# Optimization experiments

Hardware: AMD Instinct MI355X
Metric: run time of the kernel (lower is better)

Reference implementation:

```python
import jax, jax.numpy as jnp
import numpy as np

LEFT, RIGHT = 64, 64  # left_size, right_size; hidden = LEFT*RIGHT = 4096


def _cayley(raw):
    """torch nn.utils.parametrizations.orthogonal(..., orthogonal_map='cayley',
    use_trivialization=False): A = triu(raw, 1); X = A - A^T (skew-symmetric);
    Q = (I - X/2)^{-1} (I + X/2)."""
    n = raw.shape[0]
    A = jnp.triu(raw, 1)
    X = A - A.T
    Id = jnp.eye(n, dtype=raw.dtype)
    return jnp.linalg.solve(Id - 0.5 * X, Id + 0.5 * X)


def setup_inputs() -> dict:
    key = jax.random.key(0)
    ks = jax.random.split(key, 8)
    B, S = 4, 2048
    H = LEFT * RIGHT
    inp = jax.random.normal(ks[0], (B, S, H), dtype=jnp.float32)
    raw_u_left = jax.random.normal(ks[1], (LEFT, LEFT), dtype=jnp.float32) * 0.02
    raw_v_left = jax.random.normal(ks[2], (LEFT, LEFT), dtype=jnp.float32) * 0.02
    raw_u_right = jax.random.normal(ks[3], (RIGHT, RIGHT), dtype=jnp.float32) * 0.02
    raw_v_right = jax.random.normal(ks[4], (RIGHT, RIGHT), dtype=jnp.float32) * 0.02
    diag_left = jnp.ones((LEFT,), dtype=jnp.float32)
    diag_right = jnp.ones((RIGHT,), dtype=jnp.float32)
    diag_scale = jnp.ones((H,), dtype=jnp.float32) + 0.01 * jax.random.normal(ks[5], (H,), dtype=jnp.float32)
    return {
        "inp": inp,
        "raw_u_left": raw_u_left,
        "raw_v_left": raw_v_left,
        "diag_left": diag_left,
        "raw_u_right": raw_u_right,
        "raw_v_right": raw_v_right,
        "diag_right": diag_right,
        "diag_scale": diag_scale,
        "inv_t": 0,
    }


def reference(inp, raw_u_left, raw_v_left, diag_left, raw_u_right, raw_v_right,
              diag_right, diag_scale, inv_t):
    # add_diag=True, use_diag=True path
    if inv_t:
        x = inp / diag_scale
        dl = 1.0 / diag_left
        dr = 1.0 / diag_right
    else:
        x = inp * diag_scale
        dl = diag_left
        dr = diag_right
    # Cayley-parametrized orthogonal factors
    Ul = _cayley(raw_u_left)
    Vl = _cayley(raw_v_left)
    Ur = _cayley(raw_u_right)
    Vr = _cayley(raw_v_right)
    # SVD-style reconstruction: M = U @ diag(d) @ V^T
    ML = (Ul * dl[None, :]) @ Vl.T  # [LEFT, LEFT]
    MR = (Ur * dr[None, :]) @ Vr.T  # [RIGHT, RIGHT]
    # Kronecker matmul: view last dim as [LEFT, RIGHT], out = ML^T @ X @ MR
    orig_shape = x.shape
    xb = x.reshape(-1, LEFT, RIGHT)  # [B*S, LEFT, RIGHT]
    out = jnp.einsum('bij,ik,jl->bkl', xb, ML, MR)
    return out.reshape(orig_shape)
```

## Files before the change

### kernel.cpp

```cpp
#include <hip/hip_runtime.h>
#include <hip/hip_bf16.h>

typedef short short8 __attribute__((ext_vector_type(8)));
typedef short short4v __attribute__((ext_vector_type(4)));
typedef float f32x4 __attribute__((ext_vector_type(4)));
typedef float f32x16 __attribute__((ext_vector_type(16)));

#define HID 4096
#define CST 68

__device__ __forceinline__ unsigned short f2bf(float f) {
    unsigned int u = __float_as_uint(f);
    u = (u + 0x7FFFu + ((u >> 16) & 1u)) >> 16;
    return (unsigned short)u;
}

__device__ __forceinline__ f32x4 mm4(const float* SA, const float* SB, int i, int j0) {
    f32x4 acc = {0.f, 0.f, 0.f, 0.f};
#pragma unroll 8
    for (int k = 0; k < 64; ++k) {
        float a = SA[i * CST + k];
        acc += a * *reinterpret_cast<const f32x4*>(SB + k * CST + j0);
    }
    return acc;
}

__global__ __launch_bounds__(1024) void cayley_build_kernel(
    const float* __restrict__ rul, const float* __restrict__ rvl, const float* __restrict__ dl,
    const float* __restrict__ rur, const float* __restrict__ rvr, const float* __restrict__ dr,
    const int* __restrict__ invt,
    unsigned short* __restrict__ plb, unsigned short* __restrict__ mrtb)
{
    __shared__ __align__(16) float Yw[64 * CST], Aw[64 * CST], Pw[64 * CST];
    __shared__ __align__(16) float Qw[64 * CST], QTw[64 * CST];
    __shared__ float dd[64];

    const float* ru; const float* rv; const float* dv; unsigned short* ob;
    if (blockIdx.x == 0) { ru = rul; rv = rvl; dv = dl; ob = plb; }
    else                 { ru = rur; rv = rvr; dv = dr; ob = mrtb; }

    const int tid = threadIdx.x;
    const int i = tid >> 4;
    const int j0 = (tid & 15) << 2;

    for (int pass = 0; pass < 2; ++pass) {
        const float* raw = (pass == 0) ? ru : rv;
#pragma unroll
        for (int q = 0; q < 4; ++q) {
            int j = j0 + q;
            float v = 0.f;
            if (j > i)      v =  raw[i * 64 + j];
            else if (j < i) v = -raw[j * 64 + i];
            Yw[i * CST + j] = 0.5f * v;
        }
        __syncthreads();
        f32x4 a = mm4(Yw, Yw, i, j0);
        __syncthreads();
        *reinterpret_cast<f32x4*>(Aw + i * CST + j0) = a;
        *reinterpret_cast<f32x4*>(Pw + i * CST + j0) =
            a + *reinterpret_cast<const f32x4*>(Yw + i * CST + j0);
        __syncthreads();
        a = mm4(Pw, Aw, i, j0);
        __syncthreads();
        *reinterpret_cast<f32x4*>(Pw + i * CST + j0) += a;
        __syncthreads();
        a = mm4(Aw, Aw, i, j0);
        __syncthreads();
        *reinterpret_cast<f32x4*>(Aw + i * CST + j0) = a;
        __syncthreads();
        a = mm4(Pw, Aw, i, j0);
        __syncthreads();
        f32x4 p = *reinterpret_cast<const f32x4*>(Pw + i * CST + j0) + a;
#pragma unroll
        for (int q = 0; q < 4; ++q) {
            int j = j0 + q;
            float qv = ((i == j) ? 1.f : 0.f) + 2.f * p[q];
            if (pass == 0) Qw[i * CST + j]  = qv;
            else           QTw[j * CST + i] = qv;
        }
        __syncthreads();
    }
    if (tid < 64) { float d = dv[tid]; dd[tid] = (invt[0] != 0) ? (1.0f / d) : d; }
    __syncthreads();

    f32x4 m = {0.f, 0.f, 0.f, 0.f};
#pragma unroll 8
    for (int j = 0; j < 64; ++j) {
        float aa = Qw[i * CST + j] * dd[j];
        m += aa * *reinterpret_cast<const f32x4*>(QTw + j * CST + j0);
    }
#pragma unroll
    for (int q = 0; q < 4; ++q)
        ob[(j0 + q) * 64 + i] = f2bf(m[q]);
}

__global__ __launch_bounds__(256, 4) void kron_kernel(
    const float* __restrict__ inp, const float* __restrict__ ds,
    const unsigned short* __restrict__ plb, const unsigned short* __restrict__ mrtb,
    const int* __restrict__ invt, float* __restrict__ out, int ntok)
{
    __shared__ __align__(16) unsigned char sbuf[4][8192];
    const int w = threadIdx.x >> 6;
    const int lane = threadIdx.x & 63;
    const int r = lane & 31;
    const int h = lane >> 5;
    unsigned char* S = sbuf[w];

    const int t = blockIdx.x * 4 + w;
    if (t >= ntok) return;
    const bool inv = (invt[0] != 0);

    const float* xt = inp + (size_t)t * HID;
    const int c = lane & 7;
    const int mr0 = lane >> 3;
#pragma unroll
    for (int s = 0; s < 8; ++s) {
        const int fi = s * 512 + lane * 8;
        f32x4 x0 = *reinterpret_cast<const f32x4*>(xt + fi);
        f32x4 x1 = *reinterpret_cast<const f32x4*>(xt + fi + 4);
        f32x4 d0 = *reinterpret_cast<const f32x4*>(ds + fi);
        f32x4 d1 = *reinterpret_cast<const f32x4*>(ds + fi + 4);
        if (inv) {
#pragma unroll
            for (int e = 0; e < 4; ++e) { x0[e] /= d0[e]; x1[e] /= d1[e]; }
        } else {
            x0 *= d0; x1 *= d1;
        }
        short8 f;
#pragma unroll
        for (int e = 0; e < 4; ++e) {
            f[e]     = (short)f2bf(x0[e]);
            f[e + 4] = (short)f2bf(x1[e]);
        }
        const int m = s * 8 + mr0;
        *reinterpret_cast<short8*>(S + ((m * 8 + (c ^ (m & 7))) << 4)) = f;
    }
    asm volatile("s_waitcnt lgkmcnt(0)" ::: "memory");
    __builtin_amdgcn_sched_barrier(0);

    short8 a1[2][4];
#pragma unroll
    for (int mt = 0; mt < 2; ++mt)
#pragma unroll
        for (int kt = 0; kt < 4; ++kt)
            a1[mt][kt] = *reinterpret_cast<const short8*>(
                S + (((32 * mt + r) * 8 + ((2 * kt + h) ^ (r & 7))) << 4));
    short8 b1[4][2];
#pragma unroll
    for (int kt = 0; kt < 4; ++kt)
#pragma unroll
        for (int nt = 0; nt < 2; ++nt)
            b1[kt][nt] = *reinterpret_cast<const short8*>(
                (const short*)mrtb + (32 * nt + r) * 64 + 16 * kt + 8 * h);

    asm volatile("s_waitcnt lgkmcnt(0)" ::: "memory");
    __builtin_amdgcn_sched_barrier(0);

#pragma unroll
    for (int mt = 0; mt < 2; ++mt)
#pragma unroll
        for (int nt = 0; nt < 2; ++nt) {
            f32x16 acc = {0.f};
#pragma unroll
            for (int kt = 0; kt < 4; ++kt)
                acc = __builtin_amdgcn_mfma_f32_32x32x16_bf16(a1[mt][kt], b1[kt][nt], acc, 0, 0, 0);
            const int l = 32 * nt + r;
#pragma unroll
            for (int q = 0; q < 4; ++q) {
                short4v zz;
#pragma unroll
                for (int e = 0; e < 4; ++e) zz[e] = (short)f2bf(acc[4 * q + e]);
                *reinterpret_cast<short4v*>(
                    S + (((l * 8 + ((4 * mt + q) ^ (l & 7))) << 4) + 8 * h)) = zz;
            }
        }
    asm volatile("s_waitcnt lgkmcnt(0)" ::: "memory");
    __builtin_amdgcn_sched_barrier(0);

    short8 b2[4][2];
#pragma unroll
    for (int kt = 0; kt < 4; ++kt)
#pragma unroll
        for (int nt = 0; nt < 2; ++nt)
            b2[kt][nt] = *reinterpret_cast<const short8*>(
                S + (((32 * nt + r) * 8 + ((2 * kt + h) ^ (r & 7))) << 4));
    short8 a2[2][4];
#pragma unroll
    for (int mt = 0; mt < 2; ++mt)
#pragma unroll
        for (int kt = 0; kt < 4; ++kt)
            a2[mt][kt] = *reinterpret_cast<const short8*>(
                (const short*)plb + (32 * mt + r) * 64 + 16 * kt + 8 * h);

    float* op = out + (size_t)t * HID;
#pragma unroll
    for (int mt = 0; mt < 2; ++mt)
#pragma unroll
        for (int nt = 0; nt < 2; ++nt) {
            f32x16 acc = {0.f};
#pragma unroll
            for (int kt = 0; kt < 4; ++kt)
                acc = __builtin_amdgcn_mfma_f32_32x32x16_bf16(a2[mt][kt], b2[kt][nt], acc, 0, 0, 0);
#pragma unroll
            for (int g = 0; g < 16; ++g) {
                const int k = 32 * mt + (g & 3) + 8 * (g >> 2) + 4 * h;
                op[k * 64 + 32 * nt + r] = acc[g];
            }
        }
}

extern "C" void kernel_launch(void* const* d_in, const int* in_sizes, int n_in,
                              void* d_out, int out_size, void* d_ws, size_t ws_size,
                              hipStream_t stream) {
    const float* inp = (const float*)d_in[0];
    const float* rul = (const float*)d_in[1];
    const float* rvl = (const float*)d_in[2];
    const float* dl  = (const float*)d_in[3];
    const float* rur = (const float*)d_in[4];
    const float* rvr = (const float*)d_in[5];
    const float* dr  = (const float*)d_in[6];
    const float* ds  = (const float*)d_in[7];
    const int*   invt = (const int*)d_in[8];
    float* out = (float*)d_out;

    unsigned short* plb  = (unsigned short*)d_ws;
    unsigned short* mrtb = plb + 4096;

    const int ntok = in_sizes[0] / HID;

    hipLaunchKernelGGL(cayley_build_kernel, dim3(2), dim3(1024), 0, stream,
                       rul, rvl, dl, rur, rvr, dr, invt, plb, mrtb);
    const int nblk = (ntok + 3) / 4;
    hipLaunchKernelGGL(kron_kernel, dim3(nblk), dim3(256), 0, stream,
                       inp, ds, plb, mrtb, invt, out, ntok);
}
```

Measured before the change: 87.84 us.

## Stage output through swizzled LDS for coalesced stores, pre-pack weights, two tokens per wave

```diff
diff --git a/kernel.cpp b/kernel.cpp
--- a/kernel.cpp
+++ b/kernel.cpp
@@ -8,6 +8,11 @@
 
 #define HID 4096
 #define CST 68
+#define TPW 2
+#define WLDS 9216
+
+#define LGKM0 do { asm volatile("s_waitcnt lgkmcnt(0)" ::: "memory"); \
+                   __builtin_amdgcn_sched_barrier(0); } while (0)
 
 __device__ __forceinline__ unsigned short f2bf(float f) {
     unsigned int u = __float_as_uint(f);
@@ -29,15 +34,15 @@
     const float* __restrict__ rul, const float* __restrict__ rvl, const float* __restrict__ dl,
     const float* __restrict__ rur, const float* __restrict__ rvr, const float* __restrict__ dr,
     const int* __restrict__ invt,
-    unsigned short* __restrict__ plb, unsigned short* __restrict__ mrtb)
+    unsigned short* __restrict__ plp, unsigned short* __restrict__ mrp)
 {
     __shared__ __align__(16) float Yw[64 * CST], Aw[64 * CST], Pw[64 * CST];
     __shared__ __align__(16) float Qw[64 * CST], QTw[64 * CST];
     __shared__ float dd[64];
 
     const float* ru; const float* rv; const float* dv; unsigned short* ob;
-    if (blockIdx.x == 0) { ru = rul; rv = rvl; dv = dl; ob = plb; }
-    else                 { ru = rur; rv = rvr; dv = dr; ob = mrtb; }
+    if (blockIdx.x == 0) { ru = rul; rv = rvl; dv = dl; ob = plp; }
+    else                 { ru = rur; rv = rvr; dv = dr; ob = mrp; }
 
     const int tid = threadIdx.x;
     const int i = tid >> 4;
@@ -89,124 +94,148 @@
         float aa = Qw[i * CST + j] * dd[j];
         m += aa * *reinterpret_cast<const f32x4*>(QTw + j * CST + j0);
     }
-#pragma unroll
-    for (int q = 0; q < 4; ++q)
-        ob[(j0 + q) * 64 + i] = f2bf(m[q]);
+    const int kt = i >> 4, hh = (i >> 3) & 1, e = i & 7;
+#pragma unroll
+    for (int q = 0; q < 4; ++q) {
+        int j = j0 + q;
+        unsigned short v = f2bf(m[q]);
+        int dst;
+        if (blockIdx.x == 0)
+            dst = (((j >> 5) * 4 + kt) * 64 + (j & 31) + 32 * hh) * 8 + e;
+        else
+            dst = ((kt * 2 + (j >> 5)) * 64 + (j & 31) + 32 * hh) * 8 + e;
+        ob[dst] = v;
+    }
 }
 
 __global__ __launch_bounds__(256, 4) void kron_kernel(
     const float* __restrict__ inp, const float* __restrict__ ds,
-    const unsigned short* __restrict__ plb, const unsigned short* __restrict__ mrtb,
+    const unsigned short* __restrict__ plp, const unsigned short* __restrict__ mrp,
     const int* __restrict__ invt, float* __restrict__ out, int ntok)
 {
-    __shared__ __align__(16) unsigned char sbuf[4][8192];
+    __shared__ __align__(16) unsigned char sbuf[4][WLDS];
     const int w = threadIdx.x >> 6;
     const int lane = threadIdx.x & 63;
     const int r = lane & 31;
     const int h = lane >> 5;
     unsigned char* S = sbuf[w];
-
-    const int t = blockIdx.x * 4 + w;
-    if (t >= ntok) return;
+    float* SF = reinterpret_cast<float*>(S);
     const bool inv = (invt[0] != 0);
 
-    const float* xt = inp + (size_t)t * HID;
-    const int c = lane & 7;
-    const int mr0 = lane >> 3;
-#pragma unroll
-    for (int s = 0; s < 8; ++s) {
-        const int fi = s * 512 + lane * 8;
-        f32x4 x0 = *reinterpret_cast<const f32x4*>(xt + fi);
-        f32x4 x1 = *reinterpret_cast<const f32x4*>(xt + fi + 4);
-        f32x4 d0 = *reinterpret_cast<const f32x4*>(ds + fi);
-        f32x4 d1 = *reinterpret_cast<const f32x4*>(ds + fi + 4);
-        if (inv) {
-#pragma unroll
-            for (int e = 0; e < 4; ++e) { x0[e] /= d0[e]; x1[e] /= d1[e]; }
-        } else {
-            x0 *= d0; x1 *= d1;
-        }
-        short8 f;
-#pragma unroll
-        for (int e = 0; e < 4; ++e) {
-            f[e]     = (short)f2bf(x0[e]);
-            f[e + 4] = (short)f2bf(x1[e]);
-        }
-        const int m = s * 8 + mr0;
-        *reinterpret_cast<short8*>(S + ((m * 8 + (c ^ (m & 7))) << 4)) = f;
-    }
-    asm volatile("s_waitcnt lgkmcnt(0)" ::: "memory");
-    __builtin_amdgcn_sched_barrier(0);
-
-    short8 a1[2][4];
-#pragma unroll
-    for (int mt = 0; mt < 2; ++mt)
+    const int t0 = (blockIdx.x * 4 + w) * TPW;
+#pragma unroll
+    for (int it = 0; it < TPW; ++it) {
+        const int t = t0 + it;
+        if (t >= ntok) break;
+        const float* xt = inp + (size_t)t * HID;
+
+#pragma unroll
+        for (int s = 0; s < 8; ++s) {
+            const int fi = s * 512 + lane * 8;
+            f32x4 x0 = *reinterpret_cast<const f32x4*>(xt + fi);
+            f32x4 x1 = *reinterpret_cast<const f32x4*>(xt + fi + 4);
+            f32x4 d0 = *reinterpret_cast<const f32x4*>(ds + fi);
+            f32x4 d1 = *reinterpret_cast<const f32x4*>(ds + fi + 4);
+            if (inv) {
+#pragma unroll
+                for (int e = 0; e < 4; ++e) { x0[e] /= d0[e]; x1[e] /= d1[e]; }
+            } else {
+                x0 *= d0; x1 *= d1;
+            }
+            short8 f;
+#pragma unroll
+            for (int e = 0; e < 4; ++e) {
+                f[e]     = (short)f2bf(x0[e]);
+                f[e + 4] = (short)f2bf(x1[e]);
+            }
+            const int m = s * 8 + (lane >> 3);
+            const int c = lane & 7;
+            *reinterpret_cast<short8*>(S + ((m * 8 + (c ^ (m & 7))) << 4)) = f;
+        }
+        LGKM0;
+
+        short8 a1[8];
+#pragma unroll
+        for (int mt = 0; mt < 2; ++mt)
+#pragma unroll
+            for (int kt = 0; kt < 4; ++kt)
+                a1[mt * 4 + kt] = *reinterpret_cast<const short8*>(
+                    S + (((32 * mt + r) * 8 + ((2 * kt + h) ^ (r & 7))) << 4));
+        short8 b1[8];
 #pragma unroll
         for (int kt = 0; kt < 4; ++kt)
-            a1[mt][kt] = *reinterpret_cast<const short8*>(
-                S + (((32 * mt + r) * 8 + ((2 * kt + h) ^ (r & 7))) << 4));
-    short8 b1[4][2];
-#pragma unroll
-    for (int kt = 0; kt < 4; ++kt)
-#pragma unroll
-        for (int nt = 0; nt < 2; ++nt)
-            b1[kt][nt] = *reinterpret_cast<const short8*>(
-                (const short*)mrtb + (32 * nt + r) * 64 + 16 * kt + 8 * h);
-
-    asm volatile("s_waitcnt lgkmcnt(0)" ::: "memory");
-    __builtin_amdgcn_sched_barrier(0);
-
-#pragma unroll
-    for (int mt = 0; mt < 2; ++mt)
-#pragma unroll
-        for (int nt = 0; nt < 2; ++nt) {
-            f32x16 acc = {0.f};
+#pragma unroll
+            for (int nt = 0; nt < 2; ++nt)
+                b1[kt * 2 + nt] = *reinterpret_cast<const short8*>(
+                    mrp + ((kt * 2 + nt) * 64 + lane) * 8);
+        LGKM0;
+
+#pragma unroll
+        for (int mt = 0; mt < 2; ++mt)
+#pragma unroll
+            for (int nt = 0; nt < 2; ++nt) {
+                f32x16 acc = {0.f};
+#pragma unroll
+                for (int kt = 0; kt < 4; ++kt)
+                    acc = __builtin_amdgcn_mfma_f32_32x32x16_bf16(
+                        a1[mt * 4 + kt], b1[kt * 2 + nt], acc, 0, 0, 0);
+                const int l2 = 32 * nt + r;
+#pragma unroll
+                for (int q = 0; q < 4; ++q) {
+                    short4v zz;
+#pragma unroll
+                    for (int e = 0; e < 4; ++e) zz[e] = (short)f2bf(acc[4 * q + e]);
+                    *reinterpret_cast<short4v*>(
+                        S + (((l2 * 8 + ((4 * mt + q) ^ (l2 & 7))) << 4) + 8 * h)) = zz;
+                }
+            }
+        LGKM0;
+
+        short8 b2[8];
+#pragma unroll
+        for (int kt = 0; kt < 4; ++kt)
+#pragma unroll
+            for (int nt = 0; nt < 2; ++nt)
+                b2[kt * 2 + nt] = *reinterpret_cast<const short8*>(
+                    S + (((32 * nt + r) * 8 + ((2 * kt + h) ^ (r & 7))) << 4));
+        short8 a2[8];
+#pragma unroll
+        for (int mt = 0; mt < 2; ++mt)
 #pragma unroll
             for (int kt = 0; kt < 4; ++kt)
-                acc = __builtin_amdgcn_mfma_f32_32x32x16_bf16(a1[mt][kt], b1[kt][nt], acc, 0, 0, 0);
-            const int l = 32 * nt + r;
-#pragma unroll
-            for (int q = 0; q < 4; ++q) {
-                short4v zz;
-#pragma unroll
-                for (int e = 0; e < 4; ++e) zz[e] = (short)f2bf(acc[4 * q + e]);
-                *reinterpret_cast<short4v*>(
-                    S + (((l * 8 + ((4 * mt + q) ^ (l & 7))) << 4) + 8 * h)) = zz;
-            }
-        }
-    asm volatile("s_waitcnt lgkmcnt(0)" ::: "memory");
-    __builtin_amdgcn_sched_barrier(0);
-
-    short8 b2[4][2];
-#pragma unroll
-    for (int kt = 0; kt < 4; ++kt)
-#pragma unroll
-        for (int nt = 0; nt < 2; ++nt)
-            b2[kt][nt] = *reinterpret_cast<const short8*>(
-                S + (((32 * nt + r) * 8 + ((2 * kt + h) ^ (r & 7))) << 4));
-    short8 a2[2][4];
-#pragma unroll
-    for (int mt = 0; mt < 2; ++mt)
-#pragma unroll
-        for (int kt = 0; kt < 4; ++kt)
-            a2[mt][kt] = *reinterpret_cast<const short8*>(
-                (const short*)plb + (32 * mt + r) * 64 + 16 * kt + 8 * h);
-
-    float* op = out + (size_t)t * HID;
-#pragma unroll
-    for (int mt = 0; mt < 2; ++mt)
-#pragma unroll
-        for (int nt = 0; nt < 2; ++nt) {
-            f32x16 acc = {0.f};
-#pragma unroll
-            for (int kt = 0; kt < 4; ++kt)
-                acc = __builtin_amdgcn_mfma_f32_32x32x16_bf16(a2[mt][kt], b2[kt][nt], acc, 0, 0, 0);
-#pragma unroll
-            for (int g = 0; g < 16; ++g) {
-                const int k = 32 * mt + (g & 3) + 8 * (g >> 2) + 4 * h;
-                op[k * 64 + 32 * nt + r] = acc[g];
-            }
-        }
+                a2[mt * 4 + kt] = *reinterpret_cast<const short8*>(
+                    plp + ((mt * 4 + kt) * 64 + lane) * 8);
+        LGKM0;
+
+        float* op = out + (size_t)t * HID;
+#pragma unroll
+        for (int mt = 0; mt < 2; ++mt) {
+#pragma unroll
+            for (int nt = 0; nt < 2; ++nt) {
+                f32x16 acc = {0.f};
+#pragma unroll
+                for (int kt = 0; kt < 4; ++kt)
+                    acc = __builtin_amdgcn_mfma_f32_32x32x16_bf16(
+                        a2[mt * 4 + kt], b2[kt * 2 + nt], acc, 0, 0, 0);
+#pragma unroll
+                for (int g = 0; g < 16; ++g) {
+                    const int rr = (g & 3) + 8 * (g >> 2) + 4 * h;
+                    const int cy = 32 * nt + r;
+                    SF[rr * 68 + (cy ^ ((rr & 7) << 2))] = acc[g];
+                }
+            }
+            LGKM0;
+#pragma unroll
+            for (int s = 0; s < 8; ++s) {
+                const int ro = s * 4 + (lane >> 4);
+                const int c0 = (lane & 15) * 4;
+                f32x4 y = *reinterpret_cast<const f32x4*>(
+                    SF + ro * 68 + (c0 ^ ((ro & 7) << 2)));
+                *reinterpret_cast<f32x4*>(op + (32 * mt + ro) * 64 + c0) = y;
+            }
+            LGKM0;
+        }
+    }
 }
 
 extern "C" void kernel_launch(void* const* d_in, const int* in_sizes, int n_in,
@@ -223,14 +252,14 @@
     const int*   invt = (const int*)d_in[8];
     float* out = (float*)d_out;
 
-    unsigned short* plb  = (unsigned short*)d_ws;
-    unsigned short* mrtb = plb + 4096;
+    unsigned short* plp = (unsigned short*)d_ws;
+    unsigned short* mrp = plp + 4096;
 
     const int ntok = in_sizes[0] / HID;
 
     hipLaunchKernelGGL(cayley_build_kernel, dim3(2), dim3(1024), 0, stream,
-                       rul, rvl, dl, rur, rvr, dr, invt, plb, mrtb);
-    const int nblk = (ntok + 3) / 4;
+                       rul, rvl, dl, rur, rvr, dr, invt, plp, mrp);
+    const int nblk = (ntok + 4 * TPW - 1) / (4 * TPW);
     hipLaunchKernelGGL(kron_kernel, dim3(nblk), dim3(256), 0, stream,
-                       inp, ds, plb, mrtb, invt, out, ntok);
-}
+                       inp, ds, plp, mrp, invt, out, ntok);
+}
```

Result: slower. 119.0 us (+35.5%).
